# Kernel tuning notes

Hardware: AMD Instinct MI355X
Metric: run time of the kernel (lower is better)

## Reference

```python
import jax, jax.numpy as jnp
import numpy as np

NUM_HEADS = 16

def setup_inputs() -> dict:
    key = jax.random.key(0)
    ks = jax.random.split(key, 9)
    B, N, D = 4, 4096, 1024
    s = 1.0 / np.sqrt(D)
    return {
        "x": jax.random.normal(ks[0], (B, N, D), dtype=jnp.float32),
        "Wq": jax.random.normal(ks[1], (D, D), dtype=jnp.float32) * s,
        "bq": jnp.zeros((D,), dtype=jnp.float32),
        "Wk": jax.random.normal(ks[2], (D, D), dtype=jnp.float32) * s,
        "bk": jnp.zeros((D,), dtype=jnp.float32),
        "Wv": jax.random.normal(ks[3], (D, D), dtype=jnp.float32) * s,
        "bv": jnp.zeros((D,), dtype=jnp.float32),
        "Wp": jax.random.normal(ks[4], (D, D), dtype=jnp.float32) * s,
        "bp": jnp.zeros((D,), dtype=jnp.float32),
    }

def _split_heads(t, H):
    B, N, D = t.shape
    return t.reshape(B, N, H, D // H).transpose(0, 2, 1, 3)  # [B,H,N,hd]

def reference(x, Wq, bq, Wk, bk, Wv, bv, Wp, bp):
    H = NUM_HEADS
    q = jax.nn.elu(x @ Wq + bq) + 1.0   # elu feature map (config.elu=True)
    k = jax.nn.elu(x @ Wk + bk) + 1.0
    v = x @ Wv + bv
    q, k, v = _split_heads(q, H), _split_heads(k, H), _split_heads(v, H)
    # k^T v: [B,H,hd,hd]
    kv = jnp.einsum('bhnd,bhne->bhde', k, v)
    numerator = jnp.einsum('bhnd,bhde->bhne', q, kv)  # [B,H,N,hd]
    # adaptive normalizer: q @ sum_k
    sum_k = k.sum(axis=2)  # [B,H,hd]
    denominator = jnp.einsum('bhnd,bhd->bhn', q, sum_k)[..., None]
    y = numerator / denominator
    B, _, N, hd = y.shape
    y = y.transpose(0, 2, 1, 3).reshape(B, N, H * hd)
    return y @ Wp + bp
```

## Files before the change

### kernel.cpp

```cpp
#include <hip/hip_runtime.h>
#include <hip/hip_bf16.h>

typedef __attribute__((ext_vector_type(4))) float f32x4;
typedef __attribute__((ext_vector_type(4))) short s16x4;
typedef __attribute__((ext_vector_type(8))) short s16x8;
typedef __attribute__((ext_vector_type(8))) __bf16 bf16x8;

#define DEV static __device__ __forceinline__

DEV float bf2f(ushort u){
  unsigned x = ((unsigned)u) << 16;
  return __builtin_bit_cast(float, x);
}
DEV ushort f2bf(float f){
  unsigned x = __builtin_bit_cast(unsigned, f);
  x += 0x7fffu + ((x >> 16) & 1u);
  return (ushort)(x >> 16);
}
DEV void load_lds16(const void* g, void* l){
  __builtin_amdgcn_global_load_lds((const __attribute__((address_space(1))) void*)g,
                                   (__attribute__((address_space(3))) void*)l, 16, 0, 0);
}

__global__ __launch_bounds__(256) void k_cvt_x(const float* __restrict__ x,
                                               ushort* __restrict__ xb, int n8){
  int i = blockIdx.x * 256 + threadIdx.x;
  if (i >= n8) return;
  const f32x4* p = (const f32x4*)(x + (size_t)i * 8);
  f32x4 a = p[0], b = p[1];
  s16x8 o;
  o[0]=(short)f2bf(a[0]); o[1]=(short)f2bf(a[1]); o[2]=(short)f2bf(a[2]); o[3]=(short)f2bf(a[3]);
  o[4]=(short)f2bf(b[0]); o[5]=(short)f2bf(b[1]); o[6]=(short)f2bf(b[2]); o[7]=(short)f2bf(b[3]);
  *(s16x8*)(xb + (size_t)i * 8) = o;
}

__global__ void k_transposeW(const float* __restrict__ Wq, const float* __restrict__ Wk,
                             const float* __restrict__ Wv, const float* __restrict__ Wp,
                             ushort* __restrict__ qkvT, ushort* __restrict__ wpT){
  __shared__ float tile[32][33];
  int z = blockIdx.z;
  const float* W = (z == 0) ? Wq : (z == 1) ? Wk : (z == 2) ? Wv : Wp;
  ushort* out = (z < 3) ? (qkvT + (size_t)z * 1024 * 1024) : wpT;
  int bx = blockIdx.x * 32, by = blockIdx.y * 32;
  int tx = threadIdx.x, ty = threadIdx.y;
  #pragma unroll
  for (int j = 0; j < 32; j += 8)
    tile[ty + j][tx] = W[(size_t)(by + ty + j) * 1024 + bx + tx];
  __syncthreads();
  #pragma unroll
  for (int j = 0; j < 32; j += 8)
    out[(size_t)(bx + ty + j) * 1024 + by + tx] = f2bf(tile[tx][ty + j]);
}

template<int MODE>
__global__ __launch_bounds__(512, 1) void k_gemm(
    const ushort* __restrict__ A, const ushort* __restrict__ Bt,
    const float* __restrict__ b0, const float* __restrict__ b1, const float* __restrict__ b2,
    ushort* __restrict__ oQ, ushort* __restrict__ oK, ushort* __restrict__ oV,
    float* __restrict__ oF, int N)
{
  const int K = 1024;
  const int NT = 16;
  __shared__ ushort ldsA[2][16384];
  __shared__ ushort ldsB[2][16384];

  int wg = blockIdx.x;
  int cpx = gridDim.x >> 3;
  wg = (wg & 7) * cpx + (wg >> 3);
  int nbn = N >> 8;
  int bmi = wg / nbn, bni = wg - bmi * nbn;
  int m0 = bmi << 8, n0 = bni << 8;
  int tid = threadIdx.x, wid = tid >> 6, lane = tid & 63;
  int wr = wid >> 2, wc = wid & 3;
  int hi = lane >> 4, L = lane & 15;

  int rr = tid >> 3;
  int gaA = ((tid & 7) ^ (rr & 7)) << 3;
  int gaB = ((tid & 7) ^ ((tid >> 5) & 7)) << 3;
  const ushort* gA = A  + (size_t)(m0 + rr) * K + gaA;
  const ushort* gB = Bt + (size_t)(n0 + rr) * K + gaB;
  int ldst = wid << 10;

  int swz = (hi ^ (L & 7)) << 4;
  int arow = (wr * 128 + L) << 7;
  int brow = ((wc * 64 + L * 4)) << 7;

  f32x4 acc[8][4] = {};
  bf16x8 aX[4], aY[4], bX[4], bY[4];

  #define RD_A(SET, BASE, MH, KX)                                              \
    _Pragma("unroll")                                                          \
    for (int m = 0; m < 4; ++m)                                                \
      SET[m] = *(const bf16x8*)((BASE) + arow + (MH) * 8192 + (m << 11) + (swz ^ (KX)));
  #define RD_B(SET, BASE, KX)                                                  \
    _Pragma("unroll")                                                          \
    for (int n = 0; n < 4; ++n)                                                \
      SET[n] = *(const bf16x8*)((BASE) + brow + (n << 7) + (swz ^ (KX)));
  #define MF(MOFF, ASET, BSET)                                                 \
    __builtin_amdgcn_s_setprio(1);                                             \
    _Pragma("unroll")                                                          \
    for (int m = 0; m < 4; ++m)                                                \
      _Pragma("unroll")                                                        \
      for (int n = 0; n < 4; ++n)                                              \
        acc[m + (MOFF)][n] =                                                   \
          __builtin_amdgcn_mfma_f32_16x16x32_bf16(ASET[m], BSET[n], acc[m + (MOFF)][n], 0, 0, 0); \
    __builtin_amdgcn_s_setprio(0);

  #define ST_B0(SB, kof) load_lds16(gB + (kof),                   (SB) + ldst);
  #define ST_B1(SB, kof) load_lds16(gB + (size_t) 64 * K + (kof), (SB) + 8192  + ldst);
  #define ST_B2(SB, kof) load_lds16(gB + (size_t)128 * K + (kof), (SB) + 16384 + ldst);
  #define ST_B3(SB, kof) load_lds16(gB + (size_t)192 * K + (kof), (SB) + 24576 + ldst);
  #define ST_A0(SA, kof) load_lds16(gA + (kof),                   (SA) + ldst);
  #define ST_A2(SA, kof) load_lds16(gA + (size_t)128 * K + (kof), (SA) + 16384 + ldst);
  #define ST_A1(SA, kof) load_lds16(gA + (size_t) 64 * K + (kof), (SA) + 8192  + ldst);
  #define ST_A3(SA, kof) load_lds16(gA + (size_t)192 * K + (kof), (SA) + 24576 + ldst);

  {
    char* SA0 = (char*)&ldsA[0][0];
    char* SB0 = (char*)&ldsB[0][0];
    char* SB1 = (char*)&ldsB[1][0];
    ST_B0(SB0, 0) ST_B1(SB0, 0) ST_B2(SB0, 0) ST_B3(SB0, 0)
    ST_A0(SA0, 0) ST_A2(SA0, 0) ST_A1(SA0, 0) ST_A3(SA0, 0)
    ST_B0(SB1, 64) ST_B1(SB1, 64)
  }
  asm volatile("s_waitcnt vmcnt(4)" ::: "memory");
  __builtin_amdgcn_s_barrier();
  RD_A(aX, (const char*)&ldsA[0][0], 0, 0)
  RD_B(bX, (const char*)&ldsB[0][0], 0)

  int buf = 0;
  for (int t = 0; t < NT; ++t) {
    const char* LA = (const char*)&ldsA[buf][0];
    const char* LB = (const char*)&ldsB[buf][0];
    char* SAn = (char*)&ldsA[buf ^ 1][0];
    char* SBn = (char*)&ldsB[buf ^ 1][0];
    char* SBc = (char*)&ldsB[buf][0];
    size_t k1 = (size_t)(t + 1) << 6;
    size_t k2 = (size_t)(t + 2) << 6;
    bool st1 = (t + 1) < NT, st2 = (t + 2) < NT;

    if (st1) asm volatile("s_waitcnt vmcnt(2)" ::: "memory");
    else     asm volatile("s_waitcnt vmcnt(0)" ::: "memory");
    __builtin_amdgcn_s_barrier();
    RD_A(aY, LA, 1, 0)
    if (st1) { ST_B2(SBn, k1) ST_B3(SBn, k1) }
    __builtin_amdgcn_sched_barrier(0);
    MF(0, aX, bX)

    __builtin_amdgcn_s_barrier();
    RD_A(aX, LA, 1, 64)
    RD_B(bY, LB, 64)
    if (st1) { ST_A0(SAn, k1) ST_A2(SAn, k1) }
    __builtin_amdgcn_sched_barrier(0);
    MF(4, aY, bX)

    __builtin_amdgcn_s_barrier();
    RD_A(aY, LA, 0, 64)
    if (st1) { ST_A1(SAn, k1) ST_A3(SAn, k1) }
    __builtin_amdgcn_sched_barrier(0);
    MF(4, aX, bY)

    asm volatile("s_waitcnt vmcnt(2)" ::: "memory");
    __builtin_amdgcn_s_barrier();
    if (st1) { RD_A(aX, SAn, 0, 0) RD_B(bX, SBn, 0) }
    if (st2) { ST_B0(SBc, k2) ST_B1(SBc, k2) }
    __builtin_amdgcn_sched_barrier(0);
    MF(0, aY, bY)

    buf ^= 1;
  }
  #undef RD_A
  #undef RD_B
  #undef MF

  int row0 = m0 + wr * 128 + (hi << 2);
  int cb4 = n0 + wc * 64 + (L << 2);
  if constexpr (MODE == 0) {
    f32x4 bias; ushort* dst; bool act;
    if (cb4 < 1024)      { bias = *(const f32x4*)(b0 + cb4);          dst = oQ + cb4;          act = true;  }
    else if (cb4 < 2048) { bias = *(const f32x4*)(b1 + (cb4 - 1024)); dst = oK + (cb4 - 1024); act = true;  }
    else                 { bias = *(const f32x4*)(b2 + (cb4 - 2048)); dst = oV + (cb4 - 2048); act = false; }
    #pragma unroll
    for (int m = 0; m < 8; ++m)
      #pragma unroll
      for (int j = 0; j < 4; ++j) {
        int r = row0 + m * 16 + j;
        s16x4 w;
        #pragma unroll
        for (int n = 0; n < 4; ++n) {
          float v = acc[m][n][j] + bias[n];
          if (act) v = (v > 0.f) ? (v + 1.f) : __expf(v);
          w[n] = (short)f2bf(v);
        }
        *(s16x4*)(dst + (size_t)r * 1024) = w;
      }
  } else {
    f32x4 bias = *(const f32x4*)(b0 + cb4);
    #pragma unroll
    for (int m = 0; m < 8; ++m)
      #pragma unroll
      for (int j = 0; j < 4; ++j) {
        int r = row0 + m * 16 + j;
        f32x4 w;
        #pragma unroll
        for (int n = 0; n < 4; ++n) w[n] = acc[m][n][j] + bias[n];
        *(f32x4*)(oF + (size_t)r * 1024 + cb4) = w;
      }
  }
}

__global__ __launch_bounds__(256, 2) void k_kv(
    const ushort* __restrict__ kbuf, const ushort* __restrict__ vbuf,
    float* __restrict__ kvp, float* __restrict__ skp)
{
  __shared__ ushort tile[2][8192];
  __shared__ float red[64 * 68];
  __shared__ float skred[4][64];

  int bh = blockIdx.x >> 3, chunk = blockIdx.x & 7;
  int b = bh >> 4, h = bh & 15;
  int tid = threadIdx.x, wid = tid >> 6, lane = tid & 63;
  int d0 = (lane >> 3) << 3, e0 = (lane & 7) << 3;

  size_t gbase = ((size_t)b * 4096 + chunk * 512 + wid * 16 + (lane >> 3)) * 1024
               + h * 64 + (lane & 7) * 8;

  float acc[8][8] = {};
  float sk[8] = {};

  #define STAGE_KV(bp, c)                                                     \
  { char* base_ = (char*)&tile[bp][0] + (wid << 11);                          \
    size_t g_ = gbase + (size_t)(c) * 65536;                                  \
    load_lds16(kbuf + g_,        base_);                                      \
    load_lds16(kbuf + g_ + 8192, base_ + 1024);                               \
    load_lds16(vbuf + g_,        base_ + 8192);                               \
    load_lds16(vbuf + g_ + 8192, base_ + 9216); }

  STAGE_KV(0, 0)

  for (int c = 0; c < 8; ++c) {
    if (c + 1 < 8) {
      STAGE_KV((c + 1) & 1, c + 1)
      asm volatile("s_waitcnt vmcnt(4)" ::: "memory");
    } else {
      asm volatile("s_waitcnt vmcnt(0)" ::: "memory");
    }
    __builtin_amdgcn_s_barrier();
    const ushort* Ks = &tile[c & 1][0];
    const ushort* Vs = &tile[c & 1][4096];
    #pragma unroll
    for (int t = 0; t < 16; ++t) {
      int nn = (wid << 4) + t;
      s16x8 k8 = *(const s16x8*)(Ks + nn * 64 + d0);
      s16x8 v8 = *(const s16x8*)(Vs + nn * 64 + e0);
      float kf[8], vf[8];
      #pragma unroll
      for (int i = 0; i < 8; ++i) { kf[i] = bf2f((ushort)k8[i]); vf[i] = bf2f((ushort)v8[i]); }
      #pragma unroll
      for (int i = 0; i < 8; ++i) {
        sk[i] += kf[i];
        #pragma unroll
        for (int j = 0; j < 8; ++j) acc[i][j] += kf[i] * vf[j];
      }
    }
    __builtin_amdgcn_sched_barrier(0);
    __builtin_amdgcn_s_barrier();
  }
  #undef STAGE_KV

  for (int w = 0; w < 4; ++w) {
    if (wid == w) {
      #pragma unroll
      for (int i = 0; i < 8; ++i)
        #pragma unroll
        for (int j4 = 0; j4 < 2; ++j4) {
          f32x4 v4;
          v4[0] = acc[i][j4 * 4 + 0]; v4[1] = acc[i][j4 * 4 + 1];
          v4[2] = acc[i][j4 * 4 + 2]; v4[3] = acc[i][j4 * 4 + 3];
          float* p = &red[(d0 + i) * 68 + e0 + j4 * 4];
          if (w == 0) *(f32x4*)p = v4;
          else        { f32x4 o = *(const f32x4*)p; *(f32x4*)p = o + v4; }
        }
    }
    __syncthreads();
  }

  size_t kvbase = ((size_t)chunk * 64 + bh) * 4096;
  #pragma unroll
  for (int i = 0; i < 16; ++i) {
    int el = tid + i * 256;
    kvp[kvbase + el] = red[(el >> 6) * 68 + (el & 63)];
  }
  if ((lane & 7) == 0) {
    #pragma unroll
    for (int i = 0; i < 8; ++i) skred[wid][d0 + i] = sk[i];
  }
  __syncthreads();
  if (tid < 64) {
    float s = 0.f;
    #pragma unroll
    for (int w = 0; w < 4; ++w) s += skred[w][tid];
    skp[(((size_t)chunk * 64 + bh) << 6) + tid] = s;
  }
}

__global__ __launch_bounds__(256, 2) void k_num(
    const ushort* __restrict__ qbuf, const float* __restrict__ kvp,
    const float* __restrict__ skp, ushort* __restrict__ ybuf)
{
  __shared__ float kvs[4096];
  __shared__ float sks[64];
  int bh = blockIdx.x >> 5, ch = blockIdx.x & 31;
  int b = bh >> 4, h = bh & 15;
  int tid = threadIdx.x;
  #pragma unroll
  for (int i = 0; i < 4; ++i) {
    f32x4 s = {0.f, 0.f, 0.f, 0.f};
    #pragma unroll
    for (int sl = 0; sl < 8; ++sl)
      s += *(const f32x4*)&kvp[(((size_t)sl * 64 + bh) << 12) + ((i * 256 + tid) << 2)];
    *(f32x4*)&kvs[(i * 256 + tid) << 2] = s;
  }
  if (tid < 64) {
    float s = 0.f;
    #pragma unroll
    for (int sl = 0; sl < 8; ++sl) s += skp[(((size_t)sl * 64 + bh) << 6) + tid];
    sks[tid] = s;
  }
  __syncthreads();

  int rl = tid >> 2, eq = (tid & 3) << 4;
  size_t row0 = (size_t)b * 4096 + ch * 128 + rl;
  const ushort* q0 = qbuf + row0 * 1024 + h * 64;
  const ushort* q1 = q0 + (size_t)64 * 1024;
  s16x8 qa[8], qb[8];
  #pragma unroll
  for (int i = 0; i < 8; ++i) { qa[i] = *(const s16x8*)(q0 + i * 8); qb[i] = *(const s16x8*)(q1 + i * 8); }

  float a0[16] = {}, a1[16] = {};
  float den0 = 0.f, den1 = 0.f;
  #pragma unroll
  for (int d = 0; d < 64; ++d) {
    float x0 = bf2f((ushort)qa[d >> 3][d & 7]);
    float x1 = bf2f((ushort)qb[d >> 3][d & 7]);
    float s = sks[d];
    den0 += x0 * s; den1 += x1 * s;
    const f32x4* kr = (const f32x4*)&kvs[d * 64 + eq];
    #pragma unroll
    for (int j = 0; j < 4; ++j) {
      f32x4 k4 = kr[j];
      #pragma unroll
      for (int u = 0; u < 4; ++u) {
        a0[j * 4 + u] += x0 * k4[u];
        a1[j * 4 + u] += x1 * k4[u];
      }
    }
  }
  float i0 = 1.f / den0, i1 = 1.f / den1;
  ushort* y0 = ybuf + row0 * 1024 + h * 64 + eq;
  ushort* y1 = y0 + (size_t)64 * 1024;
  s16x8 p0[2], p1[2];
  #pragma unroll
  for (int j = 0; j < 16; ++j) {
    p0[j >> 3][j & 7] = (short)f2bf(a0[j] * i0);
    p1[j >> 3][j & 7] = (short)f2bf(a1[j] * i1);
  }
  *(s16x8*)y0 = p0[0]; *((s16x8*)y0 + 1) = p0[1];
  *(s16x8*)y1 = p1[0]; *((s16x8*)y1 + 1) = p1[1];
}

extern "C" void kernel_launch(void* const* d_in, const int* in_sizes, int n_in,
                              void* d_out, int out_size, void* d_ws, size_t ws_size,
                              hipStream_t stream)
{
  const float* x  = (const float*)d_in[0];
  const float* Wq = (const float*)d_in[1];
  const float* bq = (const float*)d_in[2];
  const float* Wk = (const float*)d_in[3];
  const float* bk = (const float*)d_in[4];
  const float* Wv = (const float*)d_in[5];
  const float* bv = (const float*)d_in[6];
  const float* Wp = (const float*)d_in[7];
  const float* bp = (const float*)d_in[8];

  char* ws = (char*)d_ws;
  ushort* xb    = (ushort*)(ws + 0);
  ushort* qkvT  = (ushort*)(ws + 33554432);
  ushort* wpT   = (ushort*)(ws + 39845888);
  ushort* ybuf  = (ushort*)(ws + 41943040);
  float*  kvp   = (float*)(ws + 0);
  float*  skp   = (float*)(ws + 8388608);

  ushort* vbuf = (ushort*)d_out;
  ushort* qbuf = (ushort*)d_out + 16777216;
  ushort* kbuf = ybuf;

  k_cvt_x<<<8192, 256, 0, stream>>>(x, xb, 2097152);
  k_transposeW<<<dim3(32, 32, 4), dim3(32, 8), 0, stream>>>(Wq, Wk, Wv, Wp, qkvT, wpT);
  k_gemm<0><<<768, 512, 0, stream>>>(xb, qkvT, bq, bk, bv, qbuf, kbuf, vbuf, nullptr, 3072);
  k_kv<<<512, 256, 0, stream>>>(kbuf, vbuf, kvp, skp);
  k_num<<<2048, 256, 0, stream>>>(qbuf, kvp, skp, ybuf);
  k_gemm<1><<<256, 512, 0, stream>>>(ybuf, wpT, bp, nullptr, nullptr,
                                     nullptr, nullptr, nullptr, (float*)d_out, 1024);
}
```

Measured before the change: 243.9 us.

## Compute numerator and denominator in k_num with bf16 MFMA instead of scalar FMAs

Rewrites the per-head q·kv and q·sum_k step to use 16x16x32 bf16 MFMA instructions. The reduced kv matrix is converted to bf16 and stored transposed in a swizzled LDS layout, and the denominator comes from an extra MFMA against the bf16 sum_k vector. The grid is reshaped to 512 blocks of 512 threads, each covering 512 rows, so the kv reduction is repeated far fewer times. The aim is to replace scalar FP32 FMAs with matrix-core throughput; kv and sum_k are now rounded to bf16, which adds precision error.

```diff
diff --git a/kernel.cpp b/kernel.cpp
--- a/kernel.cpp
+++ b/kernel.cpp
@@ -304,69 +304,78 @@
   }
 }
 
-__global__ __launch_bounds__(256, 2) void k_num(
+__global__ __launch_bounds__(512, 2) void k_num(
     const ushort* __restrict__ qbuf, const float* __restrict__ kvp,
     const float* __restrict__ skp, ushort* __restrict__ ybuf)
 {
-  __shared__ float kvs[4096];
-  __shared__ float sks[64];
-  int bh = blockIdx.x >> 5, ch = blockIdx.x & 31;
+  __shared__ float kvf[4096];
+  __shared__ ushort kvtb[4096];
+  __shared__ ushort skb[64];
+
+  int bh = blockIdx.x >> 3, chunk = blockIdx.x & 7;
   int b = bh >> 4, h = bh & 15;
-  int tid = threadIdx.x;
-  #pragma unroll
-  for (int i = 0; i < 4; ++i) {
+  int tid = threadIdx.x, wid = tid >> 6, lane = tid & 63;
+  int hi = lane >> 4, L = lane & 15;
+
+  #pragma unroll
+  for (int i = 0; i < 2; ++i) {
+    int i4 = tid + i * 512;
     f32x4 s = {0.f, 0.f, 0.f, 0.f};
     #pragma unroll
     for (int sl = 0; sl < 8; ++sl)
-      s += *(const f32x4*)&kvp[(((size_t)sl * 64 + bh) << 12) + ((i * 256 + tid) << 2)];
-    *(f32x4*)&kvs[(i * 256 + tid) << 2] = s;
+      s += *(const f32x4*)&kvp[(((size_t)sl * 64 + bh) << 12) + ((size_t)i4 << 2)];
+    *(f32x4*)&kvf[i4 << 2] = s;
   }
   if (tid < 64) {
     float s = 0.f;
     #pragma unroll
     for (int sl = 0; sl < 8; ++sl) s += skp[(((size_t)sl * 64 + bh) << 6) + tid];
-    sks[tid] = s;
+    skb[tid] = f2bf(s);
   }
   __syncthreads();
-
-  int rl = tid >> 2, eq = (tid & 3) << 4;
-  size_t row0 = (size_t)b * 4096 + ch * 128 + rl;
-  const ushort* q0 = qbuf + row0 * 1024 + h * 64;
-  const ushort* q1 = q0 + (size_t)64 * 1024;
-  s16x8 qa[8], qb[8];
-  #pragma unroll
-  for (int i = 0; i < 8; ++i) { qa[i] = *(const s16x8*)(q0 + i * 8); qb[i] = *(const s16x8*)(q1 + i * 8); }
-
-  float a0[16] = {}, a1[16] = {};
-  float den0 = 0.f, den1 = 0.f;
-  #pragma unroll
-  for (int d = 0; d < 64; ++d) {
-    float x0 = bf2f((ushort)qa[d >> 3][d & 7]);
-    float x1 = bf2f((ushort)qb[d >> 3][d & 7]);
-    float s = sks[d];
-    den0 += x0 * s; den1 += x1 * s;
-    const f32x4* kr = (const f32x4*)&kvs[d * 64 + eq];
+  {
+    int e = tid >> 3, dg = tid & 7;
+    s16x8 o;
+    #pragma unroll
+    for (int j = 0; j < 8; ++j) o[j] = (short)f2bf(kvf[(dg * 8 + j) * 64 + e]);
+    *(s16x8*)((char*)kvtb + e * 128 + ((dg ^ (e & 7)) << 4)) = o;
+  }
+  __syncthreads();
+
+  size_t r0 = (size_t)b * 4096 + chunk * 512 + wid * 64;
+  const ushort* qb = qbuf + (r0 + L) * 1024 + h * 64 + hi * 8;
+
+  f32x4 acc[4][4] = {};
+  f32x4 accd[4] = {};
+  #pragma unroll
+  for (int kk = 0; kk < 2; ++kk) {
+    bf16x8 bfr[4], bfd;
+    bfd = *(const bf16x8*)((const char*)skb + kk * 64 + hi * 16);
+    #pragma unroll
+    for (int n = 0; n < 4; ++n) {
+      int e = L * 4 + n;
+      bfr[n] = *(const bf16x8*)((char*)kvtb + e * 128 + ((((kk << 2) | hi) ^ (e & 7)) << 4));
+    }
+    #pragma unroll
+    for (int m = 0; m < 4; ++m) {
+      bf16x8 af = *(const bf16x8*)(qb + (size_t)m * 16 * 1024 + kk * 32);
+      #pragma unroll
+      for (int n = 0; n < 4; ++n)
+        acc[m][n] = __builtin_amdgcn_mfma_f32_16x16x32_bf16(af, bfr[n], acc[m][n], 0, 0, 0);
+      accd[m] = __builtin_amdgcn_mfma_f32_16x16x32_bf16(af, bfd, accd[m], 0, 0, 0);
+    }
+  }
+
+  #pragma unroll
+  for (int m = 0; m < 4; ++m)
     #pragma unroll
     for (int j = 0; j < 4; ++j) {
-      f32x4 k4 = kr[j];
-      #pragma unroll
-      for (int u = 0; u < 4; ++u) {
-        a0[j * 4 + u] += x0 * k4[u];
-        a1[j * 4 + u] += x1 * k4[u];
-      }
-    }
-  }
-  float i0 = 1.f / den0, i1 = 1.f / den1;
-  ushort* y0 = ybuf + row0 * 1024 + h * 64 + eq;
-  ushort* y1 = y0 + (size_t)64 * 1024;
-  s16x8 p0[2], p1[2];
-  #pragma unroll
-  for (int j = 0; j < 16; ++j) {
-    p0[j >> 3][j & 7] = (short)f2bf(a0[j] * i0);
-    p1[j >> 3][j & 7] = (short)f2bf(a1[j] * i1);
-  }
-  *(s16x8*)y0 = p0[0]; *((s16x8*)y0 + 1) = p0[1];
-  *(s16x8*)y1 = p1[0]; *((s16x8*)y1 + 1) = p1[1];
+      float inv = 1.0f / accd[m][j];
+      s16x4 w;
+      #pragma unroll
+      for (int n = 0; n < 4; ++n) w[n] = (short)f2bf(acc[m][n][j] * inv);
+      *(s16x4*)(ybuf + (r0 + m * 16 + hi * 4 + j) * 1024 + h * 64 + L * 4) = w;
+    }
 }
 
 extern "C" void kernel_launch(void* const* d_in, const int* in_sizes, int n_in,
@@ -399,7 +408,7 @@
   k_transposeW<<<dim3(32, 32, 4), dim3(32, 8), 0, stream>>>(Wq, Wk, Wv, Wp, qkvT, wpT);
   k_gemm<0><<<768, 512, 0, stream>>>(xb, qkvT, bq, bk, bv, qbuf, kbuf, vbuf, nullptr, 3072);
   k_kv<<<512, 256, 0, stream>>>(kbuf, vbuf, kvp, skp);
-  k_num<<<2048, 256, 0, stream>>>(qbuf, kvp, skp, ybuf);
+  k_num<<<512, 512, 0, stream>>>(qbuf, kvp, skp, ybuf);
   k_gemm<1><<<256, 512, 0, stream>>>(ybuf, wpT, bp, nullptr, nullptr,
                                      nullptr, nullptr, nullptr, (float*)d_out, 1024);
 }
```

New measurement: 236.9 us. 1.03x faster.
